# Performance work log

Hardware: AMD Instinct MI355X
Metric: run time of the kernel (lower is better)

The kernel has to match this reference:

```python
import jax, jax.numpy as jnp
import numpy as np

E, K = 8, 2              # n_routed_experts, num_experts_per_tok
H, I = 2048, 1408        # hidden_size, moe_intermediate_size
IS = 2 * I               # shared experts intermediate (n_shared_experts * I)
B, S = 2, 512


def setup_inputs() -> dict:
    key = jax.random.key(0)
    ks = jax.random.split(key, 8)
    w = 0.02
    return {
        "hidden_states": jax.random.normal(ks[0], (B, S, H), jnp.float32),
        "router_w": jax.random.normal(ks[1], (E, H), jnp.float32) * w,
        "w_gate": jax.random.normal(ks[2], (E, I, H), jnp.float32) * w,
        "w_up": jax.random.normal(ks[3], (E, I, H), jnp.float32) * w,
        "w_down": jax.random.normal(ks[4], (E, H, I), jnp.float32) * w,
        "sw_gate": jax.random.normal(ks[5], (IS, H), jnp.float32) * w,
        "sw_up": jax.random.normal(ks[6], (IS, H), jnp.float32) * w,
        "sw_down": jax.random.normal(ks[7], (H, IS), jnp.float32) * w,
    }


def reference(hidden_states, router_w, w_gate, w_up, w_down, sw_gate, sw_up, sw_down):
    b, s, h = hidden_states.shape
    x = hidden_states.reshape(-1, h)                      # [T, H]
    t = x.shape[0]

    # Router: F.linear(x, gate_weight) -> softmax (fp32) -> topk (sorted)
    router_logits = x @ router_w.T                        # [T, E]
    scores = jax.nn.softmax(router_logits.astype(jnp.float32), axis=-1)
    routing_weights, selected = jax.lax.top_k(scores, K)  # [T, K]
    routing_weights = routing_weights / (routing_weights.sum(-1, keepdims=True) + 1e-6)
    routing_weights = routing_weights.astype(x.dtype)

    # Combine weights: [T, E], zero where expert not selected (exact gather/scatter math)
    cw = jnp.zeros((t, E), x.dtype).at[jnp.arange(t)[:, None], selected].add(routing_weights)

    # Per-expert SwiGLU FFN, batched over experts (grouped GEMM form)
    g = jnp.einsum('td,eid->eti', x, w_gate)              # [E, T, I]
    u = jnp.einsum('td,eid->eti', x, w_up)                # [E, T, I]
    y = jnp.einsum('eti,edi->etd', jax.nn.silu(g) * u, w_down)  # [E, T, H]
    moe_out = jnp.einsum('etd,te->td', y, cw)             # weighted combine -> [T, H]

    # Shared experts SwiGLU over all tokens
    shared = (jax.nn.silu(x @ sw_gate.T) * (x @ sw_up.T)) @ sw_down.T  # [T, H]

    final = (moe_out + shared).reshape(b, s, h)
    return final, router_logits
```

## Files before the change

### kernel.cpp

```cpp
#include <hip/hip_runtime.h>
#include <hip/hip_bf16.h>
#include <math.h>

#define T_TOK 1024
#define HDIM  2048
#define NEXP  8
#define IDIM  1408
#define ISH   2816
#define ROW_CAP 3072
#define ROWS_ALL 4096
#define MOE_TILES 24
#define NT_TOT 32
#define ATILE (128*64)

typedef __attribute__((ext_vector_type(8))) short bf16x8;
typedef __attribute__((ext_vector_type(4))) float f32x4;

static __device__ __forceinline__ unsigned short f2bf(float f) {
  __hip_bfloat16 h = __float2bfloat16(f);
  return __builtin_bit_cast(unsigned short, h);
}

#define PIPE_WAIT(N) do { \
    asm volatile("s_waitcnt vmcnt(" #N ")" ::: "memory"); \
    __builtin_amdgcn_s_barrier(); \
    __builtin_amdgcn_sched_barrier(0); \
  } while (0)

#define RAW_BAR() do { \
    __builtin_amdgcn_s_barrier(); \
    __builtin_amdgcn_sched_barrier(0); \
  } while (0)

__global__ __launch_bounds__(256) void router_kernel(
    const float* __restrict__ x, const float* __restrict__ rw,
    float* __restrict__ logits_out, int* __restrict__ selk, float* __restrict__ cwk)
{
  int t = blockIdx.x;
  int tid = threadIdx.x;
  float part[NEXP];
  const float* xr = x + (size_t)t * HDIM + tid * 8;
  float4 xa = *reinterpret_cast<const float4*>(xr);
  float4 xb = *reinterpret_cast<const float4*>(xr + 4);
  for (int e = 0; e < NEXP; ++e) {
    const float* wp = rw + (size_t)e * HDIM + tid * 8;
    float4 wa = *reinterpret_cast<const float4*>(wp);
    float4 wb = *reinterpret_cast<const float4*>(wp + 4);
    part[e] = xa.x*wa.x + xa.y*wa.y + xa.z*wa.z + xa.w*wa.w
            + xb.x*wb.x + xb.y*wb.y + xb.z*wb.z + xb.w*wb.w;
  }
  for (int e = 0; e < NEXP; ++e)
    for (int off = 32; off; off >>= 1)
      part[e] += __shfl_xor(part[e], off, 64);
  __shared__ float sums[4][NEXP];
  int wid = tid >> 6, lane = tid & 63;
  if (lane == 0) for (int e = 0; e < NEXP; ++e) sums[wid][e] = part[e];
  __syncthreads();
  if (tid == 0) {
    float lg[NEXP];
    for (int e = 0; e < NEXP; ++e) lg[e] = sums[0][e] + sums[1][e] + sums[2][e] + sums[3][e];
    float mx = lg[0];
    for (int e = 1; e < NEXP; ++e) mx = fmaxf(mx, lg[e]);
    float p[NEXP], s = 0.f;
    for (int e = 0; e < NEXP; ++e) { p[e] = expf(lg[e] - mx); s += p[e]; }
    for (int e = 0; e < NEXP; ++e) p[e] /= s;
    int i1 = 0;
    for (int e = 1; e < NEXP; ++e) if (lg[e] > lg[i1]) i1 = e;
    int i2 = -1;
    for (int e = 0; e < NEXP; ++e) { if (e == i1) continue; if (i2 < 0 || lg[e] > lg[i2]) i2 = e; }
    float denom = p[i1] + p[i2] + 1e-6f;
    selk[t*2] = i1; selk[t*2+1] = i2;
    cwk[t*2] = p[i1] / denom; cwk[t*2+1] = p[i2] / denom;
    for (int e = 0; e < NEXP; ++e) logits_out[t * NEXP + e] = lg[e];
  }
}

__global__ __launch_bounds__(512) void plan_kernel(
    const int* __restrict__ selk, const float* __restrict__ cwk,
    int* __restrict__ rowidx, int* __restrict__ tok_of_row,
    float* __restrict__ rowwgt, int* __restrict__ tile_tab)
{
  __shared__ int cnt[NEXP];
  __shared__ int seg[NEXP];
  int tid = threadIdx.x;
  int w = tid >> 6, lane = tid & 63;
  for (int i = tid; i < ROW_CAP; i += 512) { tok_of_row[i] = -1; rowwgt[i] = 0.f; }
  for (int i = tid; i < T_TOK; i += 512) { tok_of_row[ROW_CAP + i] = i; rowwgt[ROW_CAP + i] = 1.f; }
  int total = 0;
  for (int base = 0; base < 2 * T_TOK; base += 64) {
    unsigned long long m = __ballot(selk[base + lane] == w);
    total += __popcll(m);
  }
  if (lane == 0) cnt[w] = total;
  __syncthreads();
  if (tid == 0) {
    int s = 0;
    for (int e = 0; e < NEXP; ++e) { seg[e] = s; s += (cnt[e] + 127) & ~127; }
  }
  __syncthreads();
  int run = seg[w];
  for (int base = 0; base < 2 * T_TOK; base += 64) {
    int i = base + lane;
    bool f = selk[i] == w;
    unsigned long long m = __ballot(f);
    if (f) {
      int r = run + __popcll(m & ((1ull << lane) - 1ull));
      rowidx[i] = r;
      tok_of_row[r] = i >> 1;
      rowwgt[r] = cwk[i];
    }
    run += __popcll(m);
  }
  __syncthreads();
  if (tid < NT_TOT) {
    int e = -1, valid = 0;
    if (tid < MOE_TILES) {
      int base = tid * 128;
      for (int k = 0; k < NEXP; ++k) {
        int s0 = seg[k], s1 = s0 + ((cnt[k] + 127) & ~127);
        if (base >= s0 && base < s1) {
          e = k;
          valid = cnt[k] - (base - s0);
          if (valid > 128) valid = 128;
          if (valid < 0) valid = 0;
        }
      }
    } else { e = 0; valid = 128; }
    tile_tab[tid*2] = e;
    tile_tab[tid*2+1] = valid;
  }
}

__global__ __launch_bounds__(256) void gather_kernel(
    const float* __restrict__ x, const int* __restrict__ tok_of_row,
    unsigned short* __restrict__ xg)
{
  int r = blockIdx.x;
  int tid = threadIdx.x;
  int tok = tok_of_row[r];
  unsigned short* dst = xg + (size_t)r * HDIM + tid * 8;
  union { unsigned short us[8]; uint4 q; } p;
  if (tok < 0) {
    p.q = uint4{0, 0, 0, 0};
  } else {
    const float* src = x + (size_t)tok * HDIM + tid * 8;
    float4 a = *reinterpret_cast<const float4*>(src);
    float4 b = *reinterpret_cast<const float4*>(src + 4);
    p.us[0]=f2bf(a.x); p.us[1]=f2bf(a.y); p.us[2]=f2bf(a.z); p.us[3]=f2bf(a.w);
    p.us[4]=f2bf(b.x); p.us[5]=f2bf(b.y); p.us[6]=f2bf(b.z); p.us[7]=f2bf(b.w);
  }
  *reinterpret_cast<uint4*>(dst) = p.q;
}

static __device__ __forceinline__ void cvt_row(
    const float* __restrict__ src, unsigned short* __restrict__ dst, int tid)
{
  size_t idx = (size_t)tid * 8;
  float4 va = *reinterpret_cast<const float4*>(src + idx);
  float4 vb = *reinterpret_cast<const float4*>(src + idx + 4);
  union { unsigned short us[8]; uint4 q; } p;
  p.us[0]=f2bf(va.x); p.us[1]=f2bf(va.y); p.us[2]=f2bf(va.z); p.us[3]=f2bf(va.w);
  p.us[4]=f2bf(vb.x); p.us[5]=f2bf(vb.y); p.us[6]=f2bf(vb.z); p.us[7]=f2bf(vb.w);
  *reinterpret_cast<uint4*>(dst + idx) = p.q;
}

__global__ __launch_bounds__(256) void wcvt_gu_kernel(
    const float* __restrict__ wg, const float* __restrict__ wu,
    const float* __restrict__ sg, const float* __restrict__ su,
    unsigned short* __restrict__ dmoe, unsigned short* __restrict__ dsh)
{
  int b = blockIdx.x;
  const float* src; unsigned short* dst; size_t drow;
  if (b < NEXP * IDIM) {
    int e = b / IDIM, i = b - e * IDIM;
    src = wg + (size_t)b * HDIM; dst = dmoe;
    drow = (size_t)e * 2 * IDIM + ((i >> 4) << 5) + (i & 15);
  } else if (b < 2 * NEXP * IDIM) {
    int bb = b - NEXP * IDIM;
    int e = bb / IDIM, i = bb - e * IDIM;
    src = wu + (size_t)bb * HDIM; dst = dmoe;
    drow = (size_t)e * 2 * IDIM + ((i >> 4) << 5) + 16 + (i & 15);
  } else if (b < 2 * NEXP * IDIM + ISH) {
    int i = b - 2 * NEXP * IDIM;
    src = sg + (size_t)i * HDIM; dst = dsh;
    drow = ((size_t)(i >> 4) << 5) + (i & 15);
  } else {
    int i = b - 2 * NEXP * IDIM - ISH;
    src = su + (size_t)i * HDIM; dst = dsh;
    drow = ((size_t)(i >> 4) << 5) + 16 + (i & 15);
  }
  cvt_row(src, dst + drow * HDIM, threadIdx.x);
}

__global__ __launch_bounds__(256) void wcvt_dn_kernel(
    const float* __restrict__ wd, const float* __restrict__ swd,
    unsigned short* __restrict__ dmoe, unsigned short* __restrict__ dsh,
    int nchunks_moe)
{
  int b = blockIdx.x;
  const float* s; unsigned short* d; size_t off;
  if (b < nchunks_moe) { s = wd; d = dmoe; off = (size_t)b * 2048; }
  else { s = swd; d = dsh; off = (size_t)(b - nchunks_moe) * 2048; }
  size_t idx = off + threadIdx.x * 8;
  float4 va = *reinterpret_cast<const float4*>(s + idx);
  float4 vb = *reinterpret_cast<const float4*>(s + idx + 4);
  union { unsigned short us[8]; uint4 q; } p;
  p.us[0]=f2bf(va.x); p.us[1]=f2bf(va.y); p.us[2]=f2bf(va.z); p.us[3]=f2bf(va.w);
  p.us[4]=f2bf(vb.x); p.us[5]=f2bf(vb.y); p.us[6]=f2bf(vb.z); p.us[7]=f2bf(vb.w);
  *reinterpret_cast<uint4*>(d + idx) = p.q;
}

static __device__ __forceinline__ void stage_t(
    const unsigned short* __restrict__ base, size_t ld, int k0,
    unsigned short* Ls, int wid, int lane)
{
  #pragma unroll
  for (int j = 0; j < 2; ++j) {
    int row = j * 64 + wid * 8 + (lane >> 3);
    int col = ((lane & 7) ^ (row & 7)) << 3;
    const unsigned short* src = base + (size_t)row * ld + k0 + col;
    unsigned short* dst = &Ls[(j * 64 + wid * 8) * 64];
    __builtin_amdgcn_global_load_lds(
        (const __attribute__((address_space(1))) void*)src,
        (__attribute__((address_space(3))) void*)dst, 16, 0, 0);
  }
}

__global__ __launch_bounds__(512) void gu_kernel(
    const unsigned short* __restrict__ xg,
    const unsigned short* __restrict__ wgub, const unsigned short* __restrict__ swgub,
    const float* __restrict__ rowwgt, const int* __restrict__ tile_tab,
    unsigned short* __restrict__ hg, unsigned short* __restrict__ hsh)
{
  int bid = blockIdx.x;
  int lb = (bid & 7) * 110 + (bid >> 3);
  int mt, nt;
  if (lb < MOE_TILES * 22) { mt = lb % MOE_TILES; nt = lb / MOE_TILES; }
  else { int s = lb - MOE_TILES * 22; mt = MOE_TILES + (s & 7); nt = s >> 3; }

  int e = tile_tab[mt*2], valid = tile_tab[mt*2+1];
  if (valid <= 0) return;
  bool sh = mt >= MOE_TILES;
  int m0 = mt * 128;
  const unsigned short* wb; unsigned short* hout; int ldo;
  if (sh) { wb = swgub; hout = hsh + (size_t)(m0 - ROW_CAP) * ISH; ldo = ISH; }
  else {
    wb = wgub + (size_t)e * 2 * IDIM * HDIM;
    hout = hg + (size_t)m0 * IDIM; ldo = IDIM;
  }

  __shared__ unsigned short As[2 * ATILE];
  __shared__ unsigned short Bs[2 * ATILE];

  int tid = threadIdx.x, wid = tid >> 6, lane = tid & 63;
  int wr = wid >> 2, wc = wid & 3;
  int fr = lane & 15, fq = lane >> 4, fq8 = fq << 3;

  f32x4 acc[4][2] = {{}};

  const unsigned short* abase = xg + (size_t)m0 * HDIM;
  const unsigned short* bbase = wb + (size_t)(nt * 128) * HDIM;

  stage_t(abase, HDIM, 0, As, wid, lane);
  stage_t(bbase, HDIM, 0, Bs, wid, lane);

  const int NK = HDIM / 64;
  for (int t = 0; t < NK; ++t) {
    int cur = t & 1;
    if (t + 1 < NK) {
      stage_t(abase, HDIM, (t + 1) * 64, As + (cur ^ 1) * ATILE, wid, lane);
      stage_t(bbase, HDIM, (t + 1) * 64, Bs + (cur ^ 1) * ATILE, wid, lane);
      PIPE_WAIT(4);
    } else {
      PIPE_WAIT(0);
    }
    const unsigned short* Ab = As + cur * ATILE;
    const unsigned short* Bb = Bs + cur * ATILE;
    #pragma unroll
    for (int kk = 0; kk < 64; kk += 32) {
      bf16x8 a[4], b[2];
      #pragma unroll
      for (int m = 0; m < 4; ++m) {
        int row = wr * 64 + m * 16 + fr;
        a[m] = *reinterpret_cast<const bf16x8*>(&Ab[row * 64 + ((kk + fq8) ^ ((row & 7) << 3))]);
      }
      #pragma unroll
      for (int n = 0; n < 2; ++n) {
        int brow = wc * 32 + n * 16 + fr;
        b[n] = *reinterpret_cast<const bf16x8*>(&Bb[brow * 64 + ((kk + fq8) ^ ((brow & 7) << 3))]);
      }
      #pragma unroll
      for (int m = 0; m < 4; ++m)
        #pragma unroll
        for (int n = 0; n < 2; ++n)
          acc[m][n] = __builtin_amdgcn_mfma_f32_16x16x32_bf16(a[m], b[n], acc[m][n], 0, 0, 0);
    }
    RAW_BAR();
  }

  int icol = nt * 64 + wc * 16 + fr;
  #pragma unroll
  for (int m = 0; m < 4; ++m)
    #pragma unroll
    for (int j = 0; j < 4; ++j) {
      int grow = wr * 64 + m * 16 + fq * 4 + j;
      float wv = rowwgt[m0 + grow];
      float g = acc[m][0][j], u = acc[m][1][j];
      float hv = g / (1.f + __expf(-g)) * u * wv;
      hout[(size_t)grow * ldo + icol] = f2bf(hv);
    }
}

__global__ __launch_bounds__(512) void dn_kernel(
    const unsigned short* __restrict__ hg, const unsigned short* __restrict__ hsh,
    const unsigned short* __restrict__ wdb, const unsigned short* __restrict__ swdb,
    const int* __restrict__ tile_tab,
    float* __restrict__ ydn, float* __restrict__ outf)
{
  int bid = blockIdx.x;
  int lb = (bid & 7) * 64 + (bid >> 3);
  int mt, nt;
  if (lb < MOE_TILES * 16) { mt = lb % MOE_TILES; nt = lb / MOE_TILES; }
  else { int s = lb - MOE_TILES * 16; mt = MOE_TILES + (s & 7); nt = s >> 3; }

  int e = tile_tab[mt*2], valid = tile_tab[mt*2+1];
  if (valid <= 0) return;
  bool sh = mt >= MOE_TILES;
  int m0 = mt * 128, n0 = nt * 128;
  const unsigned short* abase; const unsigned short* bbase; int K; float* obase;
  if (sh) { abase = hsh + (size_t)(m0 - ROW_CAP) * ISH; K = ISH; bbase = swdb; obase = outf + (size_t)(m0 - ROW_CAP) * HDIM; }
  else { abase = hg + (size_t)m0 * IDIM; K = IDIM; bbase = wdb + (size_t)e * HDIM * IDIM; obase = ydn + (size_t)m0 * HDIM; }

  __shared__ unsigned short As[2 * ATILE];
  __shared__ unsigned short Bs[2 * ATILE];

  int tid = threadIdx.x, wid = tid >> 6, lane = tid & 63;
  int wr = wid >> 2, wc = wid & 3;
  int fr = lane & 15, fq = lane >> 4, fq8 = fq << 3;

  f32x4 acc[4][2] = {{}};

  const unsigned short* bb = bbase + (size_t)n0 * K;

  stage_t(abase, K, 0, As, wid, lane);
  stage_t(bb,    K, 0, Bs, wid, lane);

  const int NK = K / 64;
  for (int t = 0; t < NK; ++t) {
    int cur = t & 1;
    if (t + 1 < NK) {
      stage_t(abase, K, (t + 1) * 64, As + (cur ^ 1) * ATILE, wid, lane);
      stage_t(bb,    K, (t + 1) * 64, Bs + (cur ^ 1) * ATILE, wid, lane);
      PIPE_WAIT(4);
    } else {
      PIPE_WAIT(0);
    }
    const unsigned short* Ab = As + cur * ATILE;
    const unsigned short* Bb = Bs + cur * ATILE;
    #pragma unroll
    for (int kk = 0; kk < 64; kk += 32) {
      bf16x8 a[4], b[2];
      #pragma unroll
      for (int m = 0; m < 4; ++m) {
        int row = wr * 64 + m * 16 + fr;
        a[m] = *reinterpret_cast<const bf16x8*>(&Ab[row * 64 + ((kk + fq8) ^ ((row & 7) << 3))]);
      }
      #pragma unroll
      for (int n = 0; n < 2; ++n) {
        int brow = wc * 32 + n * 16 + fr;
        b[n] = *reinterpret_cast<const bf16x8*>(&Bb[brow * 64 + ((kk + fq8) ^ ((brow & 7) << 3))]);
      }
      #pragma unroll
      for (int m = 0; m < 4; ++m)
        #pragma unroll
        for (int n = 0; n < 2; ++n)
          acc[m][n] = __builtin_amdgcn_mfma_f32_16x16x32_bf16(a[m], b[n], acc[m][n], 0, 0, 0);
    }
    RAW_BAR();
  }
  #pragma unroll
  for (int m = 0; m < 4; ++m)
    #pragma unroll
    for (int j = 0; j < 4; ++j) {
      int grow = wr * 64 + m * 16 + fq * 4 + j;
      #pragma unroll
      for (int n = 0; n < 2; ++n)
        obase[(size_t)grow * HDIM + n0 + wc * 32 + n * 16 + fr] = acc[m][n][j];
    }
}

__global__ __launch_bounds__(256) void combine_kernel(
    const float* __restrict__ ydn, const int* __restrict__ rowidx,
    float* __restrict__ outf)
{
  int t = blockIdx.x;
  int c = threadIdx.x * 8;
  int r0 = rowidx[t*2], r1 = rowidx[t*2+1];
  const float4* a0 = reinterpret_cast<const float4*>(ydn + (size_t)r0 * HDIM + c);
  const float4* a1 = reinterpret_cast<const float4*>(ydn + (size_t)r1 * HDIM + c);
  float4* o = reinterpret_cast<float4*>(outf + (size_t)t * HDIM + c);
  float4 x0 = a0[0], x1 = a0[1], y0 = a1[0], y1 = a1[1];
  float4 o0 = o[0], o1 = o[1];
  o0.x += x0.x + y0.x; o0.y += x0.y + y0.y; o0.z += x0.z + y0.z; o0.w += x0.w + y0.w;
  o1.x += x1.x + y1.x; o1.y += x1.y + y1.y; o1.z += x1.z + y1.z; o1.w += x1.w + y1.w;
  o[0] = o0; o[1] = o1;
}

extern "C" void kernel_launch(void* const* d_in, const int* in_sizes, int n_in,
                              void* d_out, int out_size, void* d_ws, size_t ws_size,
                              hipStream_t stream) {
  const float* x      = (const float*)d_in[0];
  const float* rw     = (const float*)d_in[1];
  const float* w_gate = (const float*)d_in[2];
  const float* w_up   = (const float*)d_in[3];
  const float* w_down = (const float*)d_in[4];
  const float* sw_g   = (const float*)d_in[5];
  const float* sw_u   = (const float*)d_in[6];
  const float* sw_d   = (const float*)d_in[7];
  float* out_final  = (float*)d_out;
  float* out_logits = out_final + (size_t)T_TOK * HDIM;

  char* ws = (char*)d_ws;
  int*   selk     = (int*)(ws + 0);
  float* cwk      = (float*)(ws + 8192);
  int*   rowidx   = (int*)(ws + 16384);
  int*   tokrow   = (int*)(ws + 24576);
  float* rowwgt   = (float*)(ws + 40960);
  int*   tile_tab = (int*)(ws + 57344);
  size_t off = 65536;
  unsigned short* xg  = (unsigned short*)(ws + off);  off += (size_t)ROWS_ALL * HDIM * 2;
  unsigned short* hg  = (unsigned short*)(ws + off);  off += (size_t)ROW_CAP * IDIM * 2;
  unsigned short* hsh = (unsigned short*)(ws + off);  off += (size_t)T_TOK * ISH * 2;
  float* ydn          = (float*)(ws + off);           off += (size_t)ROW_CAP * HDIM * 4;
  unsigned short* wbuf  = (unsigned short*)(ws + off);
  unsigned short* wgub  = wbuf;
  unsigned short* swgub = wgub + (size_t)NEXP * 2 * IDIM * HDIM;
  unsigned short* wdb   = wbuf;
  unsigned short* swdb  = wdb + (size_t)NEXP * HDIM * IDIM;

  router_kernel<<<T_TOK, 256, 0, stream>>>(x, rw, out_logits, selk, cwk);
  plan_kernel<<<1, 512, 0, stream>>>(selk, cwk, rowidx, tokrow, rowwgt, tile_tab);
  gather_kernel<<<ROWS_ALL, 256, 0, stream>>>(x, tokrow, xg);

  wcvt_gu_kernel<<<28160, 256, 0, stream>>>(w_gate, w_up, sw_g, sw_u, wgub, swgub);

  gu_kernel<<<880, 512, 0, stream>>>(xg, wgub, swgub, rowwgt, tile_tab, hg, hsh);

  wcvt_dn_kernel<<<14080, 256, 0, stream>>>(w_down, sw_d, wdb, swdb, 11264);

  dn_kernel<<<512, 512, 0, stream>>>(hg, hsh, wdb, swdb, tile_tab, ydn, out_final);
  combine_kernel<<<T_TOK, 256, 0, stream>>>(ydn, rowidx, out_final);
}
```

Before: 262.4 us.

## Read fp32 down weights directly in dn_kernel and fuse gather into weight prep

Removes the separate down-projection weight conversion pass: dn_kernel now stages fp32 w_down tiles into LDS and converts them to bf16 when building MFMA fragments, using a 64-wide N tile with twice the blocks. The token gather/convert kernel is merged into the gate/up weight conversion launch. This avoids writing and re-reading a bf16 copy of the down weights and one launch, at the cost of more bytes per B tile, more per-tile reads of fp32 weights, and extra conversion ALU inside the GEMM loop.

```diff
diff --git a/kernel.cpp b/kernel.cpp
--- a/kernel.cpp
+++ b/kernel.cpp
@@ -131,27 +131,6 @@
   }
 }
 
-__global__ __launch_bounds__(256) void gather_kernel(
-    const float* __restrict__ x, const int* __restrict__ tok_of_row,
-    unsigned short* __restrict__ xg)
-{
-  int r = blockIdx.x;
-  int tid = threadIdx.x;
-  int tok = tok_of_row[r];
-  unsigned short* dst = xg + (size_t)r * HDIM + tid * 8;
-  union { unsigned short us[8]; uint4 q; } p;
-  if (tok < 0) {
-    p.q = uint4{0, 0, 0, 0};
-  } else {
-    const float* src = x + (size_t)tok * HDIM + tid * 8;
-    float4 a = *reinterpret_cast<const float4*>(src);
-    float4 b = *reinterpret_cast<const float4*>(src + 4);
-    p.us[0]=f2bf(a.x); p.us[1]=f2bf(a.y); p.us[2]=f2bf(a.z); p.us[3]=f2bf(a.w);
-    p.us[4]=f2bf(b.x); p.us[5]=f2bf(b.y); p.us[6]=f2bf(b.z); p.us[7]=f2bf(b.w);
-  }
-  *reinterpret_cast<uint4*>(dst) = p.q;
-}
-
 static __device__ __forceinline__ void cvt_row(
     const float* __restrict__ src, unsigned short* __restrict__ dst, int tid)
 {
@@ -164,12 +143,32 @@
   *reinterpret_cast<uint4*>(dst + idx) = p.q;
 }
 
-__global__ __launch_bounds__(256) void wcvt_gu_kernel(
+__global__ __launch_bounds__(256) void prep_kernel(
+    const float* __restrict__ x, const int* __restrict__ tok_of_row,
+    unsigned short* __restrict__ xg,
     const float* __restrict__ wg, const float* __restrict__ wu,
     const float* __restrict__ sg, const float* __restrict__ su,
     unsigned short* __restrict__ dmoe, unsigned short* __restrict__ dsh)
 {
-  int b = blockIdx.x;
+  int blk = blockIdx.x;
+  int tid = threadIdx.x;
+  if (blk < ROWS_ALL) {
+    int tok = tok_of_row[blk];
+    unsigned short* dst = xg + (size_t)blk * HDIM + tid * 8;
+    union { unsigned short us[8]; uint4 q; } p;
+    if (tok < 0) {
+      p.q = uint4{0, 0, 0, 0};
+    } else {
+      const float* src = x + (size_t)tok * HDIM + tid * 8;
+      float4 a = *reinterpret_cast<const float4*>(src);
+      float4 b = *reinterpret_cast<const float4*>(src + 4);
+      p.us[0]=f2bf(a.x); p.us[1]=f2bf(a.y); p.us[2]=f2bf(a.z); p.us[3]=f2bf(a.w);
+      p.us[4]=f2bf(b.x); p.us[5]=f2bf(b.y); p.us[6]=f2bf(b.z); p.us[7]=f2bf(b.w);
+    }
+    *reinterpret_cast<uint4*>(dst) = p.q;
+    return;
+  }
+  int b = blk - ROWS_ALL;
   const float* src; unsigned short* dst; size_t drow;
   if (b < NEXP * IDIM) {
     int e = b / IDIM, i = b - e * IDIM;
@@ -189,25 +188,7 @@
     src = su + (size_t)i * HDIM; dst = dsh;
     drow = ((size_t)(i >> 4) << 5) + 16 + (i & 15);
   }
-  cvt_row(src, dst + drow * HDIM, threadIdx.x);
-}
-
-__global__ __launch_bounds__(256) void wcvt_dn_kernel(
-    const float* __restrict__ wd, const float* __restrict__ swd,
-    unsigned short* __restrict__ dmoe, unsigned short* __restrict__ dsh,
-    int nchunks_moe)
-{
-  int b = blockIdx.x;
-  const float* s; unsigned short* d; size_t off;
-  if (b < nchunks_moe) { s = wd; d = dmoe; off = (size_t)b * 2048; }
-  else { s = swd; d = dsh; off = (size_t)(b - nchunks_moe) * 2048; }
-  size_t idx = off + threadIdx.x * 8;
-  float4 va = *reinterpret_cast<const float4*>(s + idx);
-  float4 vb = *reinterpret_cast<const float4*>(s + idx + 4);
-  union { unsigned short us[8]; uint4 q; } p;
-  p.us[0]=f2bf(va.x); p.us[1]=f2bf(va.y); p.us[2]=f2bf(va.z); p.us[3]=f2bf(va.w);
-  p.us[4]=f2bf(vb.x); p.us[5]=f2bf(vb.y); p.us[6]=f2bf(vb.z); p.us[7]=f2bf(vb.w);
-  *reinterpret_cast<uint4*>(d + idx) = p.q;
+  cvt_row(src, dst + drow * HDIM, tid);
 }
 
 static __device__ __forceinline__ void stage_t(
@@ -224,6 +205,36 @@
         (const __attribute__((address_space(1))) void*)src,
         (__attribute__((address_space(3))) void*)dst, 16, 0, 0);
   }
+}
+
+static __device__ __forceinline__ void stage_bf(
+    const float* __restrict__ bbase, size_t ldb, int k0,
+    float* Bf, int wid, int lane)
+{
+  #pragma unroll
+  for (int j = 0; j < 2; ++j) {
+    int r = (wid * 2 + j) * 4 + (lane >> 4);
+    int c = lane & 15;
+    const float* src = bbase + (size_t)r * ldb + k0 + ((c ^ (r & 15)) << 2);
+    float* dst = &Bf[(size_t)((wid * 2 + j) * 4) * 64];
+    __builtin_amdgcn_global_load_lds(
+        (const __attribute__((address_space(1))) void*)src,
+        (__attribute__((address_space(3))) void*)dst, 16, 0, 0);
+  }
+}
+
+static __device__ __forceinline__ bf16x8 ldbf_frag(
+    const float* __restrict__ Bf, int brow, int s_log)
+{
+  int x = brow & 15;
+  int c0 = (s_log << 1) ^ x;
+  int c1 = ((s_log << 1) | 1) ^ x;
+  float4 q0 = *reinterpret_cast<const float4*>(Bf + (size_t)brow * 64 + (c0 << 2));
+  float4 q1 = *reinterpret_cast<const float4*>(Bf + (size_t)brow * 64 + (c1 << 2));
+  union { unsigned short us[8]; bf16x8 v; } r;
+  r.us[0]=f2bf(q0.x); r.us[1]=f2bf(q0.y); r.us[2]=f2bf(q0.z); r.us[3]=f2bf(q0.w);
+  r.us[4]=f2bf(q1.x); r.us[5]=f2bf(q1.y); r.us[6]=f2bf(q1.z); r.us[7]=f2bf(q1.w);
+  return r.v;
 }
 
 __global__ __launch_bounds__(512) void gu_kernel(
@@ -313,68 +324,63 @@
 
 __global__ __launch_bounds__(512) void dn_kernel(
     const unsigned short* __restrict__ hg, const unsigned short* __restrict__ hsh,
-    const unsigned short* __restrict__ wdb, const unsigned short* __restrict__ swdb,
+    const float* __restrict__ w_down, const float* __restrict__ sw_down,
     const int* __restrict__ tile_tab,
     float* __restrict__ ydn, float* __restrict__ outf)
 {
   int bid = blockIdx.x;
-  int lb = (bid & 7) * 64 + (bid >> 3);
+  int lb = (bid & 7) * 128 + (bid >> 3);
   int mt, nt;
-  if (lb < MOE_TILES * 16) { mt = lb % MOE_TILES; nt = lb / MOE_TILES; }
-  else { int s = lb - MOE_TILES * 16; mt = MOE_TILES + (s & 7); nt = s >> 3; }
+  if (lb < MOE_TILES * 32) { mt = lb % MOE_TILES; nt = lb / MOE_TILES; }
+  else { int s = lb - MOE_TILES * 32; mt = MOE_TILES + (s & 7); nt = s >> 3; }
 
   int e = tile_tab[mt*2], valid = tile_tab[mt*2+1];
   if (valid <= 0) return;
   bool sh = mt >= MOE_TILES;
-  int m0 = mt * 128, n0 = nt * 128;
-  const unsigned short* abase; const unsigned short* bbase; int K; float* obase;
-  if (sh) { abase = hsh + (size_t)(m0 - ROW_CAP) * ISH; K = ISH; bbase = swdb; obase = outf + (size_t)(m0 - ROW_CAP) * HDIM; }
-  else { abase = hg + (size_t)m0 * IDIM; K = IDIM; bbase = wdb + (size_t)e * HDIM * IDIM; obase = ydn + (size_t)m0 * HDIM; }
+  int m0 = mt * 128, n0 = nt * 64;
+  const unsigned short* abase; const float* bbase; int K; float* obase;
+  if (sh) { abase = hsh + (size_t)(m0 - ROW_CAP) * ISH; K = ISH; bbase = sw_down; obase = outf + (size_t)(m0 - ROW_CAP) * HDIM; }
+  else { abase = hg + (size_t)m0 * IDIM; K = IDIM; bbase = w_down + (size_t)e * HDIM * IDIM; obase = ydn + (size_t)m0 * HDIM; }
 
   __shared__ unsigned short As[2 * ATILE];
-  __shared__ unsigned short Bs[2 * ATILE];
+  __shared__ float Bf[2 * 64 * 64];
 
   int tid = threadIdx.x, wid = tid >> 6, lane = tid & 63;
   int wr = wid >> 2, wc = wid & 3;
   int fr = lane & 15, fq = lane >> 4, fq8 = fq << 3;
 
-  f32x4 acc[4][2] = {{}};
-
-  const unsigned short* bb = bbase + (size_t)n0 * K;
+  f32x4 acc[4] = {};
+
+  const float* bb = bbase + (size_t)n0 * K;
 
   stage_t(abase, K, 0, As, wid, lane);
-  stage_t(bb,    K, 0, Bs, wid, lane);
+  stage_bf(bb,   K, 0, Bf, wid, lane);
 
   const int NK = K / 64;
   for (int t = 0; t < NK; ++t) {
     int cur = t & 1;
     if (t + 1 < NK) {
       stage_t(abase, K, (t + 1) * 64, As + (cur ^ 1) * ATILE, wid, lane);
-      stage_t(bb,    K, (t + 1) * 64, Bs + (cur ^ 1) * ATILE, wid, lane);
+      stage_bf(bb,   K, (t + 1) * 64, Bf + (cur ^ 1) * 64 * 64, wid, lane);
       PIPE_WAIT(4);
     } else {
       PIPE_WAIT(0);
     }
     const unsigned short* Ab = As + cur * ATILE;
-    const unsigned short* Bb = Bs + cur * ATILE;
+    const float* Bb = Bf + cur * 64 * 64;
     #pragma unroll
-    for (int kk = 0; kk < 64; kk += 32) {
-      bf16x8 a[4], b[2];
+    for (int kk = 0; kk < 2; ++kk) {
+      bf16x8 a[4];
       #pragma unroll
       for (int m = 0; m < 4; ++m) {
         int row = wr * 64 + m * 16 + fr;
-        a[m] = *reinterpret_cast<const bf16x8*>(&Ab[row * 64 + ((kk + fq8) ^ ((row & 7) << 3))]);
+        a[m] = *reinterpret_cast<const bf16x8*>(
+            &Ab[row * 64 + ((kk * 32 + fq8) ^ ((row & 7) << 3))]);
       }
-      #pragma unroll
-      for (int n = 0; n < 2; ++n) {
-        int brow = wc * 32 + n * 16 + fr;
-        b[n] = *reinterpret_cast<const bf16x8*>(&Bb[brow * 64 + ((kk + fq8) ^ ((brow & 7) << 3))]);
-      }
+      bf16x8 b = ldbf_frag(Bb, wc * 16 + fr, kk * 4 + fq);
       #pragma unroll
       for (int m = 0; m < 4; ++m)
-        #pragma unroll
-        for (int n = 0; n < 2; ++n)
-          acc[m][n] = __builtin_amdgcn_mfma_f32_16x16x32_bf16(a[m], b[n], acc[m][n], 0, 0, 0);
+        acc[m] = __builtin_amdgcn_mfma_f32_16x16x32_bf16(a[m], b, acc[m], 0, 0, 0);
     }
     RAW_BAR();
   }
@@ -383,9 +389,7 @@
     #pragma unroll
     for (int j = 0; j < 4; ++j) {
       int grow = wr * 64 + m * 16 + fq * 4 + j;
-      #pragma unroll
-      for (int n = 0; n < 2; ++n)
-        obase[(size_t)grow * HDIM + n0 + wc * 32 + n * 16 + fr] = acc[m][n][j];
+      obase[(size_t)grow * HDIM + n0 + wc * 16 + fr] = acc[m][j];
     }
 }
 
@@ -432,22 +436,17 @@
   unsigned short* hg  = (unsigned short*)(ws + off);  off += (size_t)ROW_CAP * IDIM * 2;
   unsigned short* hsh = (unsigned short*)(ws + off);  off += (size_t)T_TOK * ISH * 2;
   float* ydn          = (float*)(ws + off);           off += (size_t)ROW_CAP * HDIM * 4;
-  unsigned short* wbuf  = (unsigned short*)(ws + off);
-  unsigned short* wgub  = wbuf;
+  unsigned short* wgub  = (unsigned short*)(ws + off);
   unsigned short* swgub = wgub + (size_t)NEXP * 2 * IDIM * HDIM;
-  unsigned short* wdb   = wbuf;
-  unsigned short* swdb  = wdb + (size_t)NEXP * HDIM * IDIM;
 
   router_kernel<<<T_TOK, 256, 0, stream>>>(x, rw, out_logits, selk, cwk);
   plan_kernel<<<1, 512, 0, stream>>>(selk, cwk, rowidx, tokrow, rowwgt, tile_tab);
-  gather_kernel<<<ROWS_ALL, 256, 0, stream>>>(x, tokrow, xg);
-
-  wcvt_gu_kernel<<<28160, 256, 0, stream>>>(w_gate, w_up, sw_g, sw_u, wgub, swgub);
+
+  prep_kernel<<<ROWS_ALL + 28160, 256, 0, stream>>>(
+      x, tokrow, xg, w_gate, w_up, sw_g, sw_u, wgub, swgub);
 
   gu_kernel<<<880, 512, 0, stream>>>(xg, wgub, swgub, rowwgt, tile_tab, hg, hsh);
 
-  wcvt_dn_kernel<<<14080, 256, 0, stream>>>(w_down, sw_d, wdb, swdb, 11264);
-
-  dn_kernel<<<512, 512, 0, stream>>>(hg, hsh, wdb, swdb, tile_tab, ydn, out_final);
+  dn_kernel<<<1024, 512, 0, stream>>>(hg, hsh, w_down, sw_d, tile_tab, ydn, out_final);
   combine_kernel<<<T_TOK, 256, 0, stream>>>(ydn, rowidx, out_final);
 }
```

New measurement: 291.0 us. 1.11x slower.

## Fuse gather into weight conversion and overlap down-weight conversion with gate/up GEMM

Applied to the files above, without the earlier changes.

Merges the token gather/convert kernel into the gate/up weight conversion launch, and appends the down-projection weight conversion blocks to the gate/up GEMM grid. The conversion work can then run on CUs that sit idle while the GEMM tiles execute, and two kernel launches go away. To make that safe, the down weights get their own workspace region instead of aliasing the gate/up buffer, which raises the memory footprint. The conversion blocks in the GEMM kernel use 512 threads over 4096-element chunks, and the kernel carries the GEMM's larger register and LDS allocation.

```diff
diff --git a/kernel.cpp b/kernel.cpp
--- a/kernel.cpp
+++ b/kernel.cpp
@@ -12,6 +12,9 @@
 #define MOE_TILES 24
 #define NT_TOT 32
 #define ATILE (128*64)
+#define GU_BLKS 880
+#define CVT2_MOE 5632
+#define CVT2_ALL 7040
 
 typedef __attribute__((ext_vector_type(8))) short bf16x8;
 typedef __attribute__((ext_vector_type(4))) float f32x4;
@@ -131,27 +134,6 @@
   }
 }
 
-__global__ __launch_bounds__(256) void gather_kernel(
-    const float* __restrict__ x, const int* __restrict__ tok_of_row,
-    unsigned short* __restrict__ xg)
-{
-  int r = blockIdx.x;
-  int tid = threadIdx.x;
-  int tok = tok_of_row[r];
-  unsigned short* dst = xg + (size_t)r * HDIM + tid * 8;
-  union { unsigned short us[8]; uint4 q; } p;
-  if (tok < 0) {
-    p.q = uint4{0, 0, 0, 0};
-  } else {
-    const float* src = x + (size_t)tok * HDIM + tid * 8;
-    float4 a = *reinterpret_cast<const float4*>(src);
-    float4 b = *reinterpret_cast<const float4*>(src + 4);
-    p.us[0]=f2bf(a.x); p.us[1]=f2bf(a.y); p.us[2]=f2bf(a.z); p.us[3]=f2bf(a.w);
-    p.us[4]=f2bf(b.x); p.us[5]=f2bf(b.y); p.us[6]=f2bf(b.z); p.us[7]=f2bf(b.w);
-  }
-  *reinterpret_cast<uint4*>(dst) = p.q;
-}
-
 static __device__ __forceinline__ void cvt_row(
     const float* __restrict__ src, unsigned short* __restrict__ dst, int tid)
 {
@@ -164,12 +146,32 @@
   *reinterpret_cast<uint4*>(dst + idx) = p.q;
 }
 
-__global__ __launch_bounds__(256) void wcvt_gu_kernel(
+__global__ __launch_bounds__(256) void prep_kernel(
+    const float* __restrict__ x, const int* __restrict__ tok_of_row,
+    unsigned short* __restrict__ xg,
     const float* __restrict__ wg, const float* __restrict__ wu,
     const float* __restrict__ sg, const float* __restrict__ su,
     unsigned short* __restrict__ dmoe, unsigned short* __restrict__ dsh)
 {
-  int b = blockIdx.x;
+  int blk = blockIdx.x;
+  int tid = threadIdx.x;
+  if (blk < ROWS_ALL) {
+    int tok = tok_of_row[blk];
+    unsigned short* dst = xg + (size_t)blk * HDIM + tid * 8;
+    union { unsigned short us[8]; uint4 q; } p;
+    if (tok < 0) {
+      p.q = uint4{0, 0, 0, 0};
+    } else {
+      const float* src = x + (size_t)tok * HDIM + tid * 8;
+      float4 a = *reinterpret_cast<const float4*>(src);
+      float4 b = *reinterpret_cast<const float4*>(src + 4);
+      p.us[0]=f2bf(a.x); p.us[1]=f2bf(a.y); p.us[2]=f2bf(a.z); p.us[3]=f2bf(a.w);
+      p.us[4]=f2bf(b.x); p.us[5]=f2bf(b.y); p.us[6]=f2bf(b.z); p.us[7]=f2bf(b.w);
+    }
+    *reinterpret_cast<uint4*>(dst) = p.q;
+    return;
+  }
+  int b = blk - ROWS_ALL;
   const float* src; unsigned short* dst; size_t drow;
   if (b < NEXP * IDIM) {
     int e = b / IDIM, i = b - e * IDIM;
@@ -189,25 +191,7 @@
     src = su + (size_t)i * HDIM; dst = dsh;
     drow = ((size_t)(i >> 4) << 5) + 16 + (i & 15);
   }
-  cvt_row(src, dst + drow * HDIM, threadIdx.x);
-}
-
-__global__ __launch_bounds__(256) void wcvt_dn_kernel(
-    const float* __restrict__ wd, const float* __restrict__ swd,
-    unsigned short* __restrict__ dmoe, unsigned short* __restrict__ dsh,
-    int nchunks_moe)
-{
-  int b = blockIdx.x;
-  const float* s; unsigned short* d; size_t off;
-  if (b < nchunks_moe) { s = wd; d = dmoe; off = (size_t)b * 2048; }
-  else { s = swd; d = dsh; off = (size_t)(b - nchunks_moe) * 2048; }
-  size_t idx = off + threadIdx.x * 8;
-  float4 va = *reinterpret_cast<const float4*>(s + idx);
-  float4 vb = *reinterpret_cast<const float4*>(s + idx + 4);
-  union { unsigned short us[8]; uint4 q; } p;
-  p.us[0]=f2bf(va.x); p.us[1]=f2bf(va.y); p.us[2]=f2bf(va.z); p.us[3]=f2bf(va.w);
-  p.us[4]=f2bf(vb.x); p.us[5]=f2bf(vb.y); p.us[6]=f2bf(vb.z); p.us[7]=f2bf(vb.w);
-  *reinterpret_cast<uint4*>(d + idx) = p.q;
+  cvt_row(src, dst + drow * HDIM, tid);
 }
 
 static __device__ __forceinline__ void stage_t(
@@ -226,14 +210,31 @@
   }
 }
 
-__global__ __launch_bounds__(512) void gu_kernel(
+__global__ __launch_bounds__(512) void gu_cvt_kernel(
     const unsigned short* __restrict__ xg,
     const unsigned short* __restrict__ wgub, const unsigned short* __restrict__ swgub,
     const float* __restrict__ rowwgt, const int* __restrict__ tile_tab,
-    unsigned short* __restrict__ hg, unsigned short* __restrict__ hsh)
-{
-  int bid = blockIdx.x;
-  int lb = (bid & 7) * 110 + (bid >> 3);
+    unsigned short* __restrict__ hg, unsigned short* __restrict__ hsh,
+    const float* __restrict__ w_down, const float* __restrict__ sw_down,
+    unsigned short* __restrict__ wdb, unsigned short* __restrict__ swdb)
+{
+  int bid0 = blockIdx.x;
+  if (bid0 >= GU_BLKS) {
+    int b = bid0 - GU_BLKS;
+    const float* s; unsigned short* d; size_t off;
+    if (b < CVT2_MOE) { s = w_down; d = wdb; off = (size_t)b * 4096; }
+    else { s = sw_down; d = swdb; off = (size_t)(b - CVT2_MOE) * 4096; }
+    size_t idx = off + (size_t)threadIdx.x * 8;
+    float4 va = *reinterpret_cast<const float4*>(s + idx);
+    float4 vb = *reinterpret_cast<const float4*>(s + idx + 4);
+    union { unsigned short us[8]; uint4 q; } p;
+    p.us[0]=f2bf(va.x); p.us[1]=f2bf(va.y); p.us[2]=f2bf(va.z); p.us[3]=f2bf(va.w);
+    p.us[4]=f2bf(vb.x); p.us[5]=f2bf(vb.y); p.us[6]=f2bf(vb.z); p.us[7]=f2bf(vb.w);
+    *reinterpret_cast<uint4*>(d + idx) = p.q;
+    return;
+  }
+
+  int lb = (bid0 & 7) * 110 + (bid0 >> 3);
   int mt, nt;
   if (lb < MOE_TILES * 22) { mt = lb % MOE_TILES; nt = lb / MOE_TILES; }
   else { int s = lb - MOE_TILES * 22; mt = MOE_TILES + (s & 7); nt = s >> 3; }
@@ -432,21 +433,19 @@
   unsigned short* hg  = (unsigned short*)(ws + off);  off += (size_t)ROW_CAP * IDIM * 2;
   unsigned short* hsh = (unsigned short*)(ws + off);  off += (size_t)T_TOK * ISH * 2;
   float* ydn          = (float*)(ws + off);           off += (size_t)ROW_CAP * HDIM * 4;
-  unsigned short* wbuf  = (unsigned short*)(ws + off);
-  unsigned short* wgub  = wbuf;
-  unsigned short* swgub = wgub + (size_t)NEXP * 2 * IDIM * HDIM;
-  unsigned short* wdb   = wbuf;
-  unsigned short* swdb  = wdb + (size_t)NEXP * HDIM * IDIM;
+  unsigned short* wgub  = (unsigned short*)(ws + off); off += (size_t)NEXP * 2 * IDIM * HDIM * 2;
+  unsigned short* swgub = (unsigned short*)(ws + off); off += (size_t)2 * ISH * HDIM * 2;
+  unsigned short* wdb   = (unsigned short*)(ws + off); off += (size_t)NEXP * HDIM * IDIM * 2;
+  unsigned short* swdb  = (unsigned short*)(ws + off);
 
   router_kernel<<<T_TOK, 256, 0, stream>>>(x, rw, out_logits, selk, cwk);
   plan_kernel<<<1, 512, 0, stream>>>(selk, cwk, rowidx, tokrow, rowwgt, tile_tab);
-  gather_kernel<<<ROWS_ALL, 256, 0, stream>>>(x, tokrow, xg);
-
-  wcvt_gu_kernel<<<28160, 256, 0, stream>>>(w_gate, w_up, sw_g, sw_u, wgub, swgub);
-
-  gu_kernel<<<880, 512, 0, stream>>>(xg, wgub, swgub, rowwgt, tile_tab, hg, hsh);
-
-  wcvt_dn_kernel<<<14080, 256, 0, stream>>>(w_down, sw_d, wdb, swdb, 11264);
+
+  prep_kernel<<<ROWS_ALL + 28160, 256, 0, stream>>>(
+      x, tokrow, xg, w_gate, w_up, sw_g, sw_u, wgub, swgub);
+
+  gu_cvt_kernel<<<GU_BLKS + CVT2_ALL, 512, 0, stream>>>(
+      xg, wgub, swgub, rowwgt, tile_tab, hg, hsh, w_down, sw_d, wdb, swdb);
 
   dn_kernel<<<512, 512, 0, stream>>>(hg, hsh, wdb, swdb, tile_tab, ydn, out_final);
   combine_kernel<<<T_TOK, 256, 0, stream>>>(ydn, rowidx, out_final);
```

New measurement: 259.7 us. Within noise of the previous version (-1.0%).
